# Kernel tuning notes

Hardware: AMD Instinct MI355X
Metric: run time of the kernel (lower is better)

Reference implementation:

```python
import jax, jax.numpy as jnp
import numpy as np

B, S, D, H = 4, 1024, 1024, 16
HD = D // H  # head_dim = 64
MASKED_BIAS = -10000.0


def setup_inputs() -> dict:
    key = jax.random.key(0)
    ks = jax.random.split(key, 7)
    sc = 0.02
    return {
        "hidden_states": jax.random.normal(ks[0], (B, S, D), jnp.float32),
        "textual_key": jax.random.normal(ks[1], (B, H, S, HD), jnp.float32),
        "textual_value": jax.random.normal(ks[2], (B, H, S, HD), jnp.float32),
        "Wc": jax.random.normal(ks[3], (D, 3 * D), jnp.float32) * sc,  # Conv1D c_attn
        "bc": jnp.zeros((3 * D,), jnp.float32),
        "Wp": jax.random.normal(ks[4], (D, D), jnp.float32) * sc,  # Conv1D c_proj
        "bp": jnp.zeros((D,), jnp.float32),
    }


def reference(hidden_states, textual_key, textual_value, Wc, bc, Wp, bp):
    b, s, d = hidden_states.shape
    # Conv1D: x @ W + b, then split into q, k, v
    qkv = hidden_states @ Wc + bc  # [B,S,3D]
    q, k, v = jnp.split(qkv, 3, axis=-1)

    def split_heads(t):  # [B,S,D] -> [B,H,S,HD]
        return t.reshape(b, s, H, HD).transpose(0, 2, 1, 3)

    q, k, v = split_heads(q), split_heads(k), split_heads(v)

    # cross-key scores against textual past + fused elementwise self-term
    text_w = jnp.einsum("bhqd,bhkd->bhqk", q, textual_key)  # [B,H,S,S_kv]
    self_w = jnp.sum(q * k, axis=-1, keepdims=True)  # [B,H,S,1]
    attn_w = jnp.concatenate([text_w, self_w], axis=-1) / (HD ** 0.5)

    # nonResidual causal mask: bias[kl-ql:kl, 1:kl+1] (strict lower-tri since
    # columns are shifted by 1) concatenated with an always-true self column
    i = jnp.arange(s)
    causal = i[None, :] < i[:, None]  # [S,S_kv]: allow k < q (strict)
    mask = jnp.concatenate([causal, jnp.ones((s, 1), bool)], axis=-1)[None, None]
    attn_w = jnp.where(mask, attn_w, jnp.asarray(MASKED_BIAS, attn_w.dtype))
    attn_w = jax.nn.softmax(attn_w, axis=-1)

    w_rest, w_self = attn_w[..., :-1], attn_w[..., -1:]
    out = jnp.einsum("bhqk,bhkd->bhqd", w_rest, textual_value) + w_self * v

    out = out.transpose(0, 2, 1, 3).reshape(b, s, d)  # merge heads
    return out @ Wp + bp
```

## Files before the change

kernel.cpp:

```cpp
#include <hip/hip_runtime.h>

typedef __bf16 bf16_t;
typedef __bf16 bf16x8 __attribute__((ext_vector_type(8)));
typedef __bf16 bf16x4 __attribute__((ext_vector_type(4)));
typedef _Float16 f16x4 __attribute__((ext_vector_type(4)));
typedef _Float16 f16x8 __attribute__((ext_vector_type(8)));
typedef float f32x4 __attribute__((ext_vector_type(4)));

__device__ __forceinline__ void gl_lds16(const void* g, void* l) {
  __builtin_amdgcn_global_load_lds(
      (const __attribute__((address_space(1))) unsigned int*)g,
      (__attribute__((address_space(3))) unsigned int*)l, 16, 0, 0);
}

__global__ __launch_bounds__(256) void prep_kernel(
    const float* __restrict__ hs, const float* __restrict__ tk, const float* __restrict__ tv,
    const float* __restrict__ Wc, const float* __restrict__ Wp,
    bf16_t* __restrict__ Ahs, bf16_t* __restrict__ Ktb, _Float16* __restrict__ Vtb,
    bf16_t* __restrict__ WcT, bf16_t* __restrict__ WpT) {
  const int blk = blockIdx.x;
  const int tid = threadIdx.x;
  if (blk < 4096) {
    const float4* src = (blk < 2048) ? (const float4*)hs : (const float4*)tk;
    bf16x8* dst = (blk < 2048) ? (bf16x8*)Ahs : (bf16x8*)Ktb;
    int i = (blk & 2047) * 256 + tid;
    float4 v0 = src[2 * i], v1 = src[2 * i + 1];
    bf16x8 o;
    o[0] = (bf16_t)v0.x; o[1] = (bf16_t)v0.y; o[2] = (bf16_t)v0.z; o[3] = (bf16_t)v0.w;
    o[4] = (bf16_t)v1.x; o[5] = (bf16_t)v1.y; o[6] = (bf16_t)v1.z; o[7] = (bf16_t)v1.w;
    dst[i] = o;
  } else {
    __shared__ float tile[32][65];
    const float* in; bf16_t* out; int C, r0, c0; size_t base = 0; bool isV = false;
    if (blk < 5632) {
      int t = blk - 4096; in = Wc; out = WcT; C = 3072;
      r0 = (t / 96) * 64; c0 = (t % 96) * 32;
    } else if (blk < 6144) {
      int t = blk - 5632; in = Wp; out = WpT; C = 1024;
      r0 = (t >> 5) * 64; c0 = (t & 31) * 32;
    } else {
      int t = blk - 6144; int z = t >> 5, rest = t & 31;
      in = tv; out = nullptr; isV = true; C = 64; base = (size_t)z * 65536;
      r0 = (rest >> 1) * 64; c0 = (rest & 1) * 32;
    }
    {
      int rr = tid >> 2, cq = (tid & 3) << 3;
      const float* sp = in + base + (size_t)(r0 + rr) * C + c0 + cq;
      float4 v0 = *(const float4*)sp, v1 = *(const float4*)(sp + 4);
      tile[cq + 0][rr] = v0.x; tile[cq + 1][rr] = v0.y;
      tile[cq + 2][rr] = v0.z; tile[cq + 3][rr] = v0.w;
      tile[cq + 4][rr] = v1.x; tile[cq + 5][rr] = v1.y;
      tile[cq + 6][rr] = v1.z; tile[cq + 7][rr] = v1.w;
    }
    __syncthreads();
    int y = tid >> 3, l = tid & 7;
    if (isV) {
      f16x8 o;
#pragma unroll
      for (int j = 0; j < 8; j++) {
        int k = ((l & 4) << 3) | ((j & 4) << 2) | ((l & 2) << 2) | ((l & 1) << 2) | (j & 3);
        o[j] = (_Float16)tile[y][k];
      }
      *(f16x8*)(Vtb + base + (size_t)(c0 + y) * 1024 + r0 + (l << 3)) = o;
    } else {
      const float* rowp = &tile[y][l << 3];
      bf16x8 o;
#pragma unroll
      for (int j = 0; j < 8; j++) o[j] = (bf16_t)rowp[j];
      *(bf16x8*)(out + (size_t)(c0 + y) * 1024 + r0 + (l << 3)) = o;
    }
  }
}

#define ATTN_M 12.0f
__global__ __launch_bounds__(512, 4) void fused_attn_kernel(
    const bf16_t* __restrict__ Ahs, const bf16_t* __restrict__ WcT,
    const float* __restrict__ bc,
    const bf16_t* __restrict__ Ktxt, const _Float16* __restrict__ VtxtT,
    bf16_t* __restrict__ Aout) {
  const int bh = blockIdx.x;
  const int y = blockIdx.y;
  const int q = (y < 4) ? y : 11 - y;
  const int qlo = q, qhi = 15 - q;
  const int b = bh >> 4, h = bh & 15;
  const int tid = threadIdx.x, wave = tid >> 6, lane = tid & 63;
  const int c = lane & 15, qd = lane >> 4;
  const int i_base = (wave < 4) ? qlo * 64 + wave * 16 : qhi * 64 + (wave & 3) * 16;
  const int kt_max = qhi;

  const bf16_t* Ktb = Ktxt + (size_t)bh * 65536;
  const _Float16* Vtb = VtxtT + (size_t)bh * 65536;

  __shared__ __align__(16) char pool[49152];
  bf16_t* Asm = (bf16_t*)pool;
  bf16_t* Bsm = (bf16_t*)(pool + 16384);
  bf16_t* Qsm = (bf16_t*)pool;
  bf16_t* KsmB = (bf16_t*)(pool + 16384);
  _Float16* VsmB = (_Float16*)(pool + 32768);

  f32x4 acc[12];
#pragma unroll
  for (int j = 0; j < 12; j++) acc[j] = (f32x4){0.f, 0.f, 0.f, 0.f};

  for (int kt = 0; kt < 16; kt++) {
#pragma unroll
    for (int p = 0; p < 2; p++) {
      int chunk = p * 512 + tid;
      int row = chunk >> 3, sb = chunk & 7, kb = sb ^ (row & 7);
      int grow = b * 1024 + ((row < 64) ? qlo * 64 + row : qhi * 64 + (row - 64));
      gl_lds16(Ahs + (size_t)grow * 1024 + kt * 64 + kb * 8, Asm + chunk * 8);
    }
#pragma unroll
    for (int p = 0; p < 3; p++) {
      int chunk = p * 512 + tid;
      int brow = chunk >> 3, sb = chunk & 7, kb = sb ^ (brow & 7);
      int wrow = (brow >> 6) * 1024 + h * 64 + (brow & 63);
      gl_lds16(WcT + (size_t)wrow * 1024 + kt * 64 + kb * 8, Bsm + chunk * 8);
    }
    __syncthreads();
#pragma unroll
    for (int kk = 0; kk < 2; kk++) {
      int arow = wave * 16 + c;
      bf16x8 af = *(const bf16x8*)(&Asm[arow * 64 + (((4 * kk + qd) ^ (arow & 7)) << 3)]);
#pragma unroll
      for (int j = 0; j < 12; j++) {
        int brow = 16 * j + c;
        bf16x8 bf = *(const bf16x8*)(&Bsm[brow * 64 + (((4 * kk + qd) ^ (brow & 7)) << 3)]);
        acc[j] = __builtin_amdgcn_mfma_f32_16x16x32_bf16(af, bf, acc[j], 0, 0, 0);
      }
    }
    __syncthreads();
  }

  {
    int row = tid >> 3, sb = tid & 7, kb = sb ^ (row & 7);
    gl_lds16(Ktb + (size_t)row * 64 + kb * 8, KsmB + tid * 8);
    gl_lds16(Vtb + (size_t)row * 1024 + kb * 8, VsmB + tid * 8);
  }

#pragma unroll
  for (int j = 0; j < 12; j++) {
    float bv = bc[(j >> 2) * 1024 + h * 64 + 16 * (j & 3) + c];
#pragma unroll
    for (int r = 0; r < 4; r++) acc[j][r] += bv;
  }

  float wself[4];
#pragma unroll
  for (int r = 0; r < 4; r++) {
    float part = acc[0][r] * acc[4][r] + acc[1][r] * acc[5][r] +
                 acc[2][r] * acc[6][r] + acc[3][r] * acc[7][r];
#pragma unroll
    for (int mk = 1; mk < 16; mk <<= 1) part += __shfl_xor(part, mk, 64);
    wself[r] = __expf(part * 0.125f - ATTN_M);
  }

  f32x4 O[4];
#pragma unroll
  for (int u = 0; u < 4; u++)
#pragma unroll
    for (int r = 0; r < 4; r++) O[u][r] = wself[r] * acc[8 + u][r];

  bf16_t* Qw = Qsm + wave * 1024;
#pragma unroll
  for (int j = 0; j < 4; j++) {
#pragma unroll
    for (int r = 0; r < 4; r++) {
      int ql = 4 * qd + r, d = 16 * j + c;
      int ch = (d >> 3) ^ (ql & 7);
      Qw[ql * 64 + (ch << 3) + (d & 7)] = (bf16_t)acc[j][r];
    }
  }
  bf16x8 aq[2];
#pragma unroll
  for (int kk = 0; kk < 2; kk++) {
    int ch = (4 * kk + qd) ^ (c & 7);
    aq[kk] = *(const bf16x8*)(&Qw[c * 64 + (ch << 3)]);
  }

  float l_loc = 0.f;
  for (int kt = 0; kt <= kt_max; kt++) {
    __syncthreads();
    if (kt < kt_max) {
      int nb = (kt + 1) & 1;
      int row = tid >> 3, sb = tid & 7, kb = sb ^ (row & 7);
      gl_lds16(Ktb + (size_t)((kt + 1) * 64 + row) * 64 + kb * 8, KsmB + nb * 4096 + tid * 8);
      gl_lds16(Vtb + (size_t)row * 1024 + (kt + 1) * 64 + kb * 8, VsmB + nb * 4096 + tid * 8);
    }
    if (64 * kt >= i_base + 16) continue;
    const bf16_t* Ks = KsmB + (kt & 1) * 4096;
    const _Float16* Vs = VsmB + (kt & 1) * 4096;

    f32x4 sc[4];
#pragma unroll
    for (int t = 0; t < 4; t++) sc[t] = (f32x4){0.f, 0.f, 0.f, 0.f};
    __builtin_amdgcn_s_setprio(1);
#pragma unroll
    for (int kk = 0; kk < 2; kk++) {
#pragma unroll
      for (int t = 0; t < 4; t++) {
        int row = 16 * t + c;
        bf16x8 bk = *(const bf16x8*)(&Ks[row * 64 + (((4 * kk + qd) ^ (row & 7)) << 3)]);
        sc[t] = __builtin_amdgcn_mfma_f32_16x16x32_bf16(bk, aq[kk], sc[t], 0, 0, 0);
      }
    }
    __builtin_amdgcn_s_setprio(0);
    const bool edge = (64 * kt + 63 >= i_base);
    f16x4 pa[4];
    if (!edge) {
#pragma unroll
      for (int t = 0; t < 4; t++)
#pragma unroll
        for (int r = 0; r < 4; r++) {
          float p = __expf(sc[t][r] * 0.125f - ATTN_M);
          l_loc += p;
          pa[t][r] = (_Float16)p;
        }
    } else {
#pragma unroll
      for (int t = 0; t < 4; t++)
#pragma unroll
        for (int r = 0; r < 4; r++) {
          bool masked = (64 * kt + 16 * t + 4 * qd + r >= i_base + c);
          float p = masked ? 0.f : __expf(sc[t][r] * 0.125f - ATTN_M);
          l_loc += p;
          pa[t][r] = (_Float16)p;
        }
    }
    __builtin_amdgcn_s_setprio(1);
#pragma unroll
    for (int tp = 0; tp < 2; tp++) {
#pragma unroll
      for (int u = 0; u < 4; u++) {
        int row = 16 * u + c;
        f16x8 vv = *(const f16x8*)(&Vs[row * 64 + (((4 * tp + qd) ^ (row & 7)) << 3)]);
        f16x4 vlo = __builtin_shufflevector(vv, vv, 0, 1, 2, 3);
        f16x4 vhi = __builtin_shufflevector(vv, vv, 4, 5, 6, 7);
        O[u] = __builtin_amdgcn_mfma_f32_16x16x16f16(pa[2 * tp], vlo, O[u], 0, 0, 0);
        O[u] = __builtin_amdgcn_mfma_f32_16x16x16f16(pa[2 * tp + 1], vhi, O[u], 0, 0, 0);
      }
    }
    __builtin_amdgcn_s_setprio(0);
  }

  l_loc += __shfl_xor(l_loc, 16, 64);
  l_loc += __shfl_xor(l_loc, 32, 64);
#pragma unroll
  for (int r = 0; r < 4; r++) {
    float lq = __shfl(l_loc, 4 * qd + r, 16);
    float inv = 1.0f / (lq + wself[r]);
    int i = i_base + 4 * qd + r;
#pragma unroll
    for (int u = 0; u < 4; u++)
      Aout[((size_t)b * 1024 + i) * 1024 + h * 64 + 16 * u + c] = (bf16_t)(O[u][r] * inv);
  }
}

__global__ __launch_bounds__(256) void gemm_out_kernel(
    const bf16_t* __restrict__ A, const bf16_t* __restrict__ Bt, const float* __restrict__ bias,
    float* __restrict__ out) {
  __shared__ bf16_t Asm[2][4096];
  __shared__ bf16_t Bsm[2][8192];
  const int tid = threadIdx.x;
  const int wave = tid >> 6, lane = tid & 63;
  const int c = lane & 15, qd = lane >> 4;
  const int wn = wave * 32;
  const int m0 = blockIdx.y * 64, n0 = blockIdx.x * 128;

  f32x4 acc[4][2];
#pragma unroll
  for (int i = 0; i < 4; i++)
#pragma unroll
    for (int j = 0; j < 2; j++) acc[i][j] = (f32x4){0.f, 0.f, 0.f, 0.f};

#pragma unroll
  for (int p = 0; p < 2; p++) {
    int chunk = p * 256 + tid;
    int row = chunk >> 3, sb = chunk & 7, kb = sb ^ (row & 7);
    gl_lds16(A + (size_t)(m0 + row) * 1024 + kb * 8, &Asm[0][chunk * 8]);
  }
#pragma unroll
  for (int p = 0; p < 4; p++) {
    int chunk = p * 256 + tid;
    int row = chunk >> 3, sb = chunk & 7, kb = sb ^ (row & 7);
    gl_lds16(Bt + (size_t)(n0 + row) * 1024 + kb * 8, &Bsm[0][chunk * 8]);
  }
  for (int it = 0; it < 16; it++) {
    __syncthreads();
    if (it < 15) {
      int nbuf = (it + 1) & 1, kt = (it + 1) * 64;
#pragma unroll
      for (int p = 0; p < 2; p++) {
        int chunk = p * 256 + tid;
        int row = chunk >> 3, sb = chunk & 7, kb = sb ^ (row & 7);
        gl_lds16(A + (size_t)(m0 + row) * 1024 + kt + kb * 8, &Asm[nbuf][chunk * 8]);
      }
#pragma unroll
      for (int p = 0; p < 4; p++) {
        int chunk = p * 256 + tid;
        int row = chunk >> 3, sb = chunk & 7, kb = sb ^ (row & 7);
        gl_lds16(Bt + (size_t)(n0 + row) * 1024 + kt + kb * 8, &Bsm[nbuf][chunk * 8]);
      }
    }
    const int bs = it & 1;
#pragma unroll
    for (int kk = 0; kk < 2; kk++) {
      bf16x8 af[4], bfr[2];
#pragma unroll
      for (int i = 0; i < 4; i++) {
        int row = 16 * i + c;
        af[i] = *(const bf16x8*)(&Asm[bs][row * 64 + (((4 * kk + qd) ^ (row & 7)) << 3)]);
      }
#pragma unroll
      for (int j = 0; j < 2; j++) {
        int row = wn + 16 * j + c;
        bfr[j] = *(const bf16x8*)(&Bsm[bs][row * 64 + (((4 * kk + qd) ^ (row & 7)) << 3)]);
      }
#pragma unroll
      for (int i = 0; i < 4; i++)
#pragma unroll
        for (int j = 0; j < 2; j++)
          acc[i][j] = __builtin_amdgcn_mfma_f32_16x16x32_bf16(af[i], bfr[j], acc[i][j], 0, 0, 0);
    }
  }
#pragma unroll
  for (int j = 0; j < 2; j++) {
    int n = n0 + wn + 16 * j + c;
    float bv = bias[n];
#pragma unroll
    for (int i = 0; i < 4; i++) {
#pragma unroll
      for (int r = 0; r < 4; r++) {
        int m = m0 + 16 * i + 4 * qd + r;
        out[(size_t)m * 1024 + n] = acc[i][j][r] + bv;
      }
    }
  }
}

extern "C" void kernel_launch(void* const* d_in, const int* in_sizes, int n_in,
                              void* d_out, int out_size, void* d_ws, size_t ws_size,
                              hipStream_t stream) {
  const float* hs = (const float*)d_in[0];
  const float* tk = (const float*)d_in[1];
  const float* tv = (const float*)d_in[2];
  const float* Wc = (const float*)d_in[3];
  const float* bc = (const float*)d_in[4];
  const float* Wp = (const float*)d_in[5];
  const float* bp = (const float*)d_in[6];
  float* out = (float*)d_out;

  bf16_t* ws = (bf16_t*)d_ws;
  const size_t M1 = 1u << 20;
  bf16_t* Ahs  = ws;
  bf16_t* WcT  = ws + 4 * M1;
  bf16_t* WpT  = ws + 7 * M1;
  bf16_t* Ktb  = ws + 8 * M1;
  _Float16* Vtb = (_Float16*)(ws + 12 * M1);
  bf16_t* Aout = ws + 28 * M1;

  prep_kernel<<<8192, 256, 0, stream>>>(hs, tk, tv, Wc, Wp, Ahs, Ktb, Vtb, WcT, WpT);
  fused_attn_kernel<<<dim3(64, 8), 512, 0, stream>>>(Ahs, WcT, bc, Ktb, Vtb, Aout);
  gemm_out_kernel<<<dim3(8, 64), 256, 0, stream>>>(Aout, WpT, bp, out);
}
```

Baseline: 172.1 us.

## Split QKV projection out of attention into a standalone tiled GEMM kernel

Moves the QKV projection out of the fused attention kernel into a separate 128x128-tiled bf16 MFMA GEMM that writes a [B*S,3D] bf16 buffer. The attention kernel then loads Q/K/V tiles from that buffer and computes the self-term dot product from LDS. Before, each attention block recomputed its slice of the projection with a 128x192 tile and poor reuse of the activation rows, and the 512-block grid was small. The cost is an extra kernel launch plus a 24MB bf16 workspace round-trip, and Q/K/V are now rounded to bf16 before the self-term.

```diff
diff --git a/kernel.cpp b/kernel.cpp
--- a/kernel.cpp
+++ b/kernel.cpp
@@ -72,10 +72,70 @@
   }
 }
 
+__global__ __launch_bounds__(256) void qkv_gemm_kernel(
+    const bf16_t* __restrict__ Ahs, const bf16_t* __restrict__ WcT,
+    const float* __restrict__ bc, bf16_t* __restrict__ Aqkv) {
+  const int bid = blockIdx.x;
+  const int swz = (bid & 7) * 96 + (bid >> 3);
+  const int bm = swz / 24, bn = swz % 24;
+  const int m0 = bm * 128, n0 = bn * 128;
+  const int tid = threadIdx.x, wave = tid >> 6, lane = tid & 63;
+  const int c = lane & 15, qd = lane >> 4;
+  const int wr = wave >> 1, wc = wave & 1;
+
+  __shared__ __align__(16) bf16_t Asm[8192];
+  __shared__ __align__(16) bf16_t Bsm[8192];
+
+  f32x4 acc[4][4];
+#pragma unroll
+  for (int i = 0; i < 4; i++)
+#pragma unroll
+    for (int j = 0; j < 4; j++) acc[i][j] = (f32x4){0.f, 0.f, 0.f, 0.f};
+
+  for (int kt = 0; kt < 16; kt++) {
+#pragma unroll
+    for (int p = 0; p < 4; p++) {
+      int chunk = p * 256 + tid;
+      int row = chunk >> 3, sb = chunk & 7, kb = sb ^ (row & 7);
+      gl_lds16(Ahs + (size_t)(m0 + row) * 1024 + kt * 64 + kb * 8, Asm + chunk * 8);
+      gl_lds16(WcT + (size_t)(n0 + row) * 1024 + kt * 64 + kb * 8, Bsm + chunk * 8);
+    }
+    __syncthreads();
+#pragma unroll
+    for (int kk = 0; kk < 2; kk++) {
+      bf16x8 af[4], bfr[4];
+#pragma unroll
+      for (int i = 0; i < 4; i++) {
+        int arow = wr * 64 + 16 * i + c;
+        af[i] = *(const bf16x8*)(&Asm[arow * 64 + (((4 * kk + qd) ^ (c & 7)) << 3)]);
+        int brow = wc * 64 + 16 * i + c;
+        bfr[i] = *(const bf16x8*)(&Bsm[brow * 64 + (((4 * kk + qd) ^ (c & 7)) << 3)]);
+      }
+#pragma unroll
+      for (int i = 0; i < 4; i++)
+#pragma unroll
+        for (int j = 0; j < 4; j++)
+          acc[i][j] = __builtin_amdgcn_mfma_f32_16x16x32_bf16(af[i], bfr[j], acc[i][j], 0, 0, 0);
+    }
+    __syncthreads();
+  }
+#pragma unroll
+  for (int j = 0; j < 4; j++) {
+    int n = n0 + wc * 64 + 16 * j + c;
+    float bv = bc[n];
+#pragma unroll
+    for (int i = 0; i < 4; i++)
+#pragma unroll
+      for (int r = 0; r < 4; r++) {
+        int m = m0 + wr * 64 + 16 * i + 4 * qd + r;
+        Aqkv[(size_t)m * 3072 + n] = (bf16_t)(acc[i][j][r] + bv);
+      }
+  }
+}
+
 #define ATTN_M 12.0f
-__global__ __launch_bounds__(512, 4) void fused_attn_kernel(
-    const bf16_t* __restrict__ Ahs, const bf16_t* __restrict__ WcT,
-    const float* __restrict__ bc,
+__global__ __launch_bounds__(512, 4) void attn_kernel(
+    const bf16_t* __restrict__ Aqkv,
     const bf16_t* __restrict__ Ktxt, const _Float16* __restrict__ VtxtT,
     bf16_t* __restrict__ Aout) {
   const int bh = blockIdx.x;
@@ -92,90 +152,68 @@
   const _Float16* Vtb = VtxtT + (size_t)bh * 65536;
 
   __shared__ __align__(16) char pool[49152];
-  bf16_t* Asm = (bf16_t*)pool;
-  bf16_t* Bsm = (bf16_t*)(pool + 16384);
   bf16_t* Qsm = (bf16_t*)pool;
+  bf16_t* Ksf = (bf16_t*)(pool + 16384);
+  bf16_t* Vsf = (bf16_t*)(pool + 32768);
   bf16_t* KsmB = (bf16_t*)(pool + 16384);
   _Float16* VsmB = (_Float16*)(pool + 32768);
 
-  f32x4 acc[12];
-#pragma unroll
-  for (int j = 0; j < 12; j++) acc[j] = (f32x4){0.f, 0.f, 0.f, 0.f};
-
-  for (int kt = 0; kt < 16; kt++) {
-#pragma unroll
-    for (int p = 0; p < 2; p++) {
-      int chunk = p * 512 + tid;
-      int row = chunk >> 3, sb = chunk & 7, kb = sb ^ (row & 7);
-      int grow = b * 1024 + ((row < 64) ? qlo * 64 + row : qhi * 64 + (row - 64));
-      gl_lds16(Ahs + (size_t)grow * 1024 + kt * 64 + kb * 8, Asm + chunk * 8);
-    }
-#pragma unroll
-    for (int p = 0; p < 3; p++) {
-      int chunk = p * 512 + tid;
-      int brow = chunk >> 3, sb = chunk & 7, kb = sb ^ (brow & 7);
-      int wrow = (brow >> 6) * 1024 + h * 64 + (brow & 63);
-      gl_lds16(WcT + (size_t)wrow * 1024 + kt * 64 + kb * 8, Bsm + chunk * 8);
-    }
-    __syncthreads();
-#pragma unroll
-    for (int kk = 0; kk < 2; kk++) {
-      int arow = wave * 16 + c;
-      bf16x8 af = *(const bf16x8*)(&Asm[arow * 64 + (((4 * kk + qd) ^ (arow & 7)) << 3)]);
-#pragma unroll
-      for (int j = 0; j < 12; j++) {
-        int brow = 16 * j + c;
-        bf16x8 bf = *(const bf16x8*)(&Bsm[brow * 64 + (((4 * kk + qd) ^ (brow & 7)) << 3)]);
-        acc[j] = __builtin_amdgcn_mfma_f32_16x16x32_bf16(af, bf, acc[j], 0, 0, 0);
-      }
-    }
-    __syncthreads();
-  }
+#pragma unroll
+  for (int sgp = 0; sgp < 6; sgp++) {
+    int seg = sgp >> 1, p = sgp & 1;
+    int chunk = p * 512 + tid;
+    int row = chunk >> 3, sb = chunk & 7, kb = sb ^ (row & 7);
+    int grow = b * 1024 + ((row < 64) ? qlo * 64 + row : qhi * 64 + (row - 64));
+    bf16_t* dst = (seg == 0) ? Qsm : (seg == 1) ? Ksf : Vsf;
+    gl_lds16(Aqkv + (size_t)grow * 3072 + seg * 1024 + h * 64 + kb * 8, dst + chunk * 8);
+  }
+  __syncthreads();
+
+  float dotv;
+  {
+    const int i = wave * 16 + (lane >> 2);
+    const int t = lane & 3;
+    const int ib = i & 7;
+    bf16x8 q0 = *(const bf16x8*)(&Qsm[i * 64 + (((2 * t) ^ ib) << 3)]);
+    bf16x8 q1 = *(const bf16x8*)(&Qsm[i * 64 + (((2 * t + 1) ^ ib) << 3)]);
+    bf16x8 k0 = *(const bf16x8*)(&Ksf[i * 64 + (((2 * t) ^ ib) << 3)]);
+    bf16x8 k1 = *(const bf16x8*)(&Ksf[i * 64 + (((2 * t + 1) ^ ib) << 3)]);
+    float s = 0.f;
+#pragma unroll
+    for (int e = 0; e < 8; e++) s += (float)q0[e] * (float)k0[e];
+#pragma unroll
+    for (int e = 0; e < 8; e++) s += (float)q1[e] * (float)k1[e];
+    s += __shfl_xor(s, 1, 64);
+    s += __shfl_xor(s, 2, 64);
+    dotv = s;
+  }
+  float wself[4];
+#pragma unroll
+  for (int r = 0; r < 4; r++)
+    wself[r] = __expf(__shfl(dotv, 16 * qd + 4 * r, 64) * 0.125f - ATTN_M);
+
+  f32x4 O[4];
+#pragma unroll
+  for (int u = 0; u < 4; u++)
+#pragma unroll
+    for (int r = 0; r < 4; r++) {
+      int row = wave * 16 + 4 * qd + r, col = 16 * u + c;
+      int ch = (col >> 3) ^ (row & 7);
+      O[u][r] = wself[r] * (float)Vsf[row * 64 + (ch << 3) + (col & 7)];
+    }
+
+  bf16x8 aq[2];
+#pragma unroll
+  for (int kk = 0; kk < 2; kk++) {
+    int qrow = wave * 16 + c;
+    aq[kk] = *(const bf16x8*)(&Qsm[qrow * 64 + (((4 * kk + qd) ^ (c & 7)) << 3)]);
+  }
+  __syncthreads();
 
   {
     int row = tid >> 3, sb = tid & 7, kb = sb ^ (row & 7);
     gl_lds16(Ktb + (size_t)row * 64 + kb * 8, KsmB + tid * 8);
     gl_lds16(Vtb + (size_t)row * 1024 + kb * 8, VsmB + tid * 8);
-  }
-
-#pragma unroll
-  for (int j = 0; j < 12; j++) {
-    float bv = bc[(j >> 2) * 1024 + h * 64 + 16 * (j & 3) + c];
-#pragma unroll
-    for (int r = 0; r < 4; r++) acc[j][r] += bv;
-  }
-
-  float wself[4];
-#pragma unroll
-  for (int r = 0; r < 4; r++) {
-    float part = acc[0][r] * acc[4][r] + acc[1][r] * acc[5][r] +
-                 acc[2][r] * acc[6][r] + acc[3][r] * acc[7][r];
-#pragma unroll
-    for (int mk = 1; mk < 16; mk <<= 1) part += __shfl_xor(part, mk, 64);
-    wself[r] = __expf(part * 0.125f - ATTN_M);
-  }
-
-  f32x4 O[4];
-#pragma unroll
-  for (int u = 0; u < 4; u++)
-#pragma unroll
-    for (int r = 0; r < 4; r++) O[u][r] = wself[r] * acc[8 + u][r];
-
-  bf16_t* Qw = Qsm + wave * 1024;
-#pragma unroll
-  for (int j = 0; j < 4; j++) {
-#pragma unroll
-    for (int r = 0; r < 4; r++) {
-      int ql = 4 * qd + r, d = 16 * j + c;
-      int ch = (d >> 3) ^ (ql & 7);
-      Qw[ql * 64 + (ch << 3) + (d & 7)] = (bf16_t)acc[j][r];
-    }
-  }
-  bf16x8 aq[2];
-#pragma unroll
-  for (int kk = 0; kk < 2; kk++) {
-    int ch = (4 * kk + qd) ^ (c & 7);
-    aq[kk] = *(const bf16x8*)(&Qw[c * 64 + (ch << 3)]);
   }
 
   float l_loc = 0.f;
@@ -357,9 +395,11 @@
   bf16_t* WpT  = ws + 7 * M1;
   bf16_t* Ktb  = ws + 8 * M1;
   _Float16* Vtb = (_Float16*)(ws + 12 * M1);
+  bf16_t* Aqkv = ws + 16 * M1;
   bf16_t* Aout = ws + 28 * M1;
 
   prep_kernel<<<8192, 256, 0, stream>>>(hs, tk, tv, Wc, Wp, Ahs, Ktb, Vtb, WcT, WpT);
-  fused_attn_kernel<<<dim3(64, 8), 512, 0, stream>>>(Ahs, WcT, bc, Ktb, Vtb, Aout);
+  qkv_gemm_kernel<<<768, 256, 0, stream>>>(Ahs, WcT, bc, Aqkv);
+  attn_kernel<<<dim3(64, 8), 512, 0, stream>>>(Aqkv, Ktb, Vtb, Aout);
   gemm_out_kernel<<<dim3(8, 64), 256, 0, stream>>>(Aout, WpT, bp, out);
 }
```

New measurement: 195.3 us. +13.5%, slower.
